# Kernel tuning notes

Measured on AMD Instinct MI355X. Metric: run time of the kernel, lower is better.

## Reference

```python
import jax, jax.numpy as jnp
import numpy as np

BN_EPS = 1e-5

def conv1d(x, w, b, pad):
    # x: (B, C_in, L), w: (C_out, C_in, K=4), stride 1
    y = jax.lax.conv_general_dilated(x, w, window_strides=(1,), padding=[(pad, pad)],
                                     dimension_numbers=('NCH', 'OIH', 'NCH'))
    return y + b[None, :, None]

def batchnorm_train(x, g, be):
    # training-mode BN over (N, L) per channel, biased variance (torch semantics)
    m = jnp.mean(x, axis=(0, 2), keepdims=True)
    v = jnp.mean((x - m) ** 2, axis=(0, 2), keepdims=True)
    return (x - m) * jax.lax.rsqrt(v + BN_EPS) * g[None, :, None] + be[None, :, None]

def setup_inputs() -> dict:
    key = jax.random.key(0)
    ks = jax.random.split(key, 12)
    B, T, C_in, E, K = 32, 4096, 12, 256, 1024
    d = {}
    d['x'] = jax.random.normal(ks[0], (B, T, C_in), jnp.float32)
    d['w1'] = jax.random.normal(ks[1], (E, C_in, 4), jnp.float32) * 0.1
    d['b1'] = jax.random.normal(ks[2], (E,), jnp.float32) * 0.1
    d['g1'] = jnp.ones((E,), jnp.float32); d['be1'] = jnp.zeros((E,), jnp.float32)
    d['w2'] = jax.random.normal(ks[3], (E, E, 4), jnp.float32) * 0.05
    d['b2'] = jax.random.normal(ks[4], (E,), jnp.float32) * 0.1
    d['g2'] = jnp.ones((E,), jnp.float32); d['be2'] = jnp.zeros((E,), jnp.float32)
    d['w3'] = jax.random.normal(ks[5], (E, E, 4), jnp.float32) * 0.05
    d['b3'] = jax.random.normal(ks[6], (E,), jnp.float32) * 0.1
    d['g3'] = jnp.ones((E,), jnp.float32); d['be3'] = jnp.zeros((E,), jnp.float32)
    d['w4'] = jax.random.normal(ks[7], (E, E, 4), jnp.float32) * 0.05
    d['b4'] = jax.random.normal(ks[8], (E,), jnp.float32) * 0.1
    d['codebook'] = jax.random.normal(ks[9], (K, E), jnp.float32)
    return d

def reference(x, w1, b1, g1, be1, w2, b2, g2, be2, w3, b3, g3, be3, w4, b4, codebook):
    h = jnp.transpose(x, (0, 2, 1))                 # (B, C, T)
    h = jax.nn.relu(batchnorm_train(conv1d(h, w1, b1, 2), g1, be1))  # (B,E,T+1)
    h = jax.nn.relu(batchnorm_train(conv1d(h, w2, b2, 1), g2, be2))  # (B,E,T)
    h = jax.nn.relu(batchnorm_train(conv1d(h, w3, b3, 2), g3, be3))  # (B,E,T+1)
    h = conv1d(h, w4, b4, 1)                                         # (B,E,T)
    z_e = jnp.transpose(h, (0, 2, 1))               # (B, T, E)
    # squared-L2 nearest codebook entry (argmin identical to cdist p=2)
    d2 = (jnp.sum(z_e ** 2, axis=-1, keepdims=True)
          - 2.0 * jnp.einsum('bte,ke->btk', z_e, codebook)
          + jnp.sum(codebook ** 2, axis=-1)[None, None, :])
    ids = jnp.argmin(d2, axis=-1)                   # (B, T) int
    z_q = codebook[ids]                             # gather (B, T, E)
    z_q = z_e + jax.lax.stop_gradient(z_q - z_e)    # straight-through
    return (z_e, z_q)
```

## Files before the change

### kernel.cpp

```cpp
#include <hip/hip_runtime.h>
#include <hip/hip_bf16.h>


#define B_   32
#define T_   4096
#define E_   256
#define CIN_ 12
#define LM_  4096

typedef __attribute__((ext_vector_type(4))) float f32x4;
typedef __attribute__((ext_vector_type(8))) short bf16x8;
typedef __attribute__((ext_vector_type(8))) unsigned short u16x8;

__device__ __forceinline__ unsigned int bf_rne(float v) {
  unsigned int u = __float_as_uint(v);
  return (u + 0x7fffu + ((u >> 16) & 1u)) >> 16;
}
__device__ __forceinline__ void split2(float v, unsigned short& h, unsigned short& l) {
  unsigned int hu = bf_rne(v);
  h = (unsigned short)hu;
  l = (unsigned short)bf_rne(v - __uint_as_float(hu << 16));
}
__device__ __forceinline__ void split3(float v, unsigned short& a,
                                       unsigned short& b, unsigned short& c) {
  unsigned int h = bf_rne(v);
  a = (unsigned short)h;
  float r1 = v - __uint_as_float(h << 16);
  unsigned int m = bf_rne(r1);
  b = (unsigned short)m;
  float r2 = r1 - __uint_as_float(m << 16);
  c = (unsigned short)bf_rne(r2);
}

__global__ __launch_bounds__(256) void prep_w_kernel(
    const float* __restrict__ w, unsigned short* __restrict__ wh,
    unsigned short* __restrict__ wm, unsigned short* __restrict__ wl) {
  const int g = blockIdx.x * 256 + threadIdx.x;
  const int coff  = g & 31;
  const int e     = (g >> 5) & 255;
  const int slice = g >> 13;
  const int cc = slice >> 2, kt = slice & 3;
  const int c = cc * 32 + coff;
  unsigned short h, m, l;
  split3(w[(size_t)e * 1024 + (size_t)c * 4 + kt], h, m, l);
  const size_t o = (size_t)slice * 8192 + (size_t)e * 32 + coff;
  wh[o] = h; wm[o] = m; wl[o] = l;
}

__global__ __launch_bounds__(256) void conv1_kernel(
    const float* __restrict__ x, const float* __restrict__ w1,
    const float* __restrict__ b1, float* __restrict__ out_main,
    float* __restrict__ out_tail) {
  __shared__ __align__(16) float xs[259][12];
  __shared__ __align__(16) float wsh[E_ * 48];
  __shared__ float bs[E_];
  const int tid = threadIdx.x;
  const int b = blockIdx.y;
  const int l0 = blockIdx.x * 256;
  for (int idx = tid; idx < 259 * 12; idx += 256) {
    int r = idx / 12, c = idx - r * 12;
    int t = l0 - 2 + r;
    xs[r][c] = (t >= 0 && t < T_) ? x[((size_t)b * T_ + t) * CIN_ + c] : 0.f;
  }
  for (int idx = tid; idx < E_ * 48; idx += 256) wsh[idx] = w1[idx];
  bs[tid] = b1[tid];
  __syncthreads();
  float xr[4][12];
  #pragma unroll
  for (int r = 0; r < 4; ++r)
    #pragma unroll
    for (int c = 0; c < 12; ++c) xr[r][c] = xs[tid + r][c];
  const int l = l0 + tid;
  for (int e = 0; e < E_; ++e) {
    float acc = bs[e];
    #pragma unroll
    for (int c = 0; c < 12; ++c) {
      const float4 wv = *(const float4*)&wsh[e * 48 + c * 4];
      acc += wv.x * xr[0][c] + wv.y * xr[1][c] + wv.z * xr[2][c] + wv.w * xr[3][c];
    }
    if (l < LM_)       out_main[((size_t)b * E_ + e) * LM_ + l] = acc;
    else if (l == LM_) out_tail[(size_t)b * E_ + e] = acc;
  }
}

__global__ __launch_bounds__(256) void bn_pass1(
    const float* __restrict__ hmain, const float* __restrict__ htail,
    float* __restrict__ psum, float* __restrict__ psq) {
  const int bx = blockIdx.x;
  const int c = bx >> 3, sl = bx & 7;
  const int tid = threadIdx.x;
  float s = 0.f, s2 = 0.f;
  for (int b = 0; b < B_; ++b) {
    const float* p = hmain + ((size_t)b * E_ + c) * LM_ + sl * 512;
    const float v0 = p[tid], v1 = p[tid + 256];
    s += v0 + v1;
    s2 += v0 * v0 + v1 * v1;
  }
  if (htail && sl == 7 && tid < B_) {
    const float v = htail[(size_t)tid * E_ + c];
    s += v; s2 += v * v;
  }
  __shared__ float sh[256], sh2[256];
  sh[tid] = s; sh2[tid] = s2; __syncthreads();
  for (int off = 128; off > 0; off >>= 1) {
    if (tid < off) { sh[tid] += sh[tid + off]; sh2[tid] += sh2[tid + off]; }
    __syncthreads();
  }
  if (tid == 0) { psum[bx] = sh[0]; psq[bx] = sh2[0]; }
}

__global__ __launch_bounds__(256) void bn_pass2(
    const float* __restrict__ psum, const float* __restrict__ psq,
    const float* __restrict__ g, const float* __restrict__ be,
    float* __restrict__ scale, float* __restrict__ shift, int hasTail) {
  const int c = threadIdx.x;
  double s = 0.0, s2 = 0.0;
  #pragma unroll
  for (int i = 0; i < 8; ++i) { s += psum[c * 8 + i]; s2 += psq[c * 8 + i]; }
  double N = (double)B_ * (double)(LM_ + hasTail);
  double m = s / N, var = s2 / N - m * m;
  double a = (double)g[c] / sqrt(var + 1e-5);
  scale[c] = (float)a;
  shift[c] = (float)((double)be[c] - m * a);
}

template <int MODE>
__global__ __launch_bounds__(256) void conv_mfma(
    const float* __restrict__ in_main, const float* __restrict__ in_tail,
    const unsigned short* __restrict__ wh, const unsigned short* __restrict__ wm,
    const unsigned short* __restrict__ wl, const float* __restrict__ bias,
    const float* __restrict__ scale, const float* __restrict__ shift,
    float* __restrict__ out, float* __restrict__ out_tail, int pad) {
  __shared__ __align__(16) char Xb[2][3][8448];
  __shared__ float sc_sh[E_], sf_sh[E_];
  const int tid = threadIdx.x, lane = tid & 63, wv = tid >> 6;
  const int q = lane >> 4, n16 = lane & 15;
  const int b = blockIdx.z, e0 = blockIdx.y * 128, l0 = blockIdx.x * 128;
  const int eB = e0 + (wv & 1) * 64;
  const int lB = (wv >> 1) * 64;
  sc_sh[tid] = scale[tid]; sf_sh[tid] = shift[tid];

  f32x4 acc[4][4];
  #pragma unroll
  for (int i = 0; i < 4; ++i)
    #pragma unroll
    for (int j = 0; j < 4; ++j) acc[i][j] = (f32x4){0.f, 0.f, 0.f, 0.f};

  const float* inb = in_main + (size_t)b * E_ * LM_;
  const float* intb = in_tail ? (in_tail + (size_t)b * E_) : nullptr;

  auto loadTask = [&](int idx, int cc, f32x4& va, f32x4& vb) {
    const int cp = idx & 15, uq = idx >> 4;
    const int c = cc * 32 + cp * 2;
    const int u0 = uq * 4;
    const int lb = l0 - pad + u0;
    const float* pa = inb + (size_t)c * LM_;
    const float* pb = pa + LM_;
    if (lb >= 0 && lb + 3 < LM_) {
      va = *(const f32x4*)(pa + lb);
      vb = *(const f32x4*)(pb + lb);
    } else {
      #pragma unroll
      for (int s = 0; s < 4; ++s) {
        const int l = lb + s;
        float oa = 0.f, ob = 0.f;
        if (l >= 0 && l < LM_)        { oa = pa[l]; ob = pb[l]; }
        else if (l == LM_ && intb)    { oa = intb[c]; ob = intb[c + 1]; }
        va[s] = oa; vb[s] = ob;
      }
    }
  };
  auto writeTask = [&](int idx, int cc, f32x4 va, f32x4 vb, int nb) {
    const int cp = idx & 15, uq = idx >> 4;
    const int c = cc * 32 + cp * 2;
    const int u0 = uq * 4;
    const int lb = l0 - pad + u0;
    const float sca = sc_sh[c], sfa = sf_sh[c];
    const float scb = sc_sh[c + 1], sfb = sf_sh[c + 1];
    const int cg = cp >> 2;
    const int cb4 = (cp & 3) * 4;
    #pragma unroll
    for (int s = 0; s < 4; ++s) {
      const int l = lb + s;
      const bool ok = (l >= 0) && (l < LM_ || (l == LM_ && intb));
      const float fa = ok ? fmaxf(fmaf(va[s], sca, sfa), 0.f) : 0.f;
      const float fb = ok ? fmaxf(fmaf(vb[s], scb, sfb), 0.f) : 0.f;
      unsigned short ha, ma, la, hb, mb, lb2;
      split3(fa, ha, ma, la);
      split3(fb, hb, mb, lb2);
      const int u = u0 + s;
      const int off = u * 64 + ((cg ^ ((u >> 1) & 3)) << 4) + cb4;
      *(unsigned int*)(Xb[nb][0] + off) = (unsigned int)ha | ((unsigned int)hb << 16);
      *(unsigned int*)(Xb[nb][1] + off) = (unsigned int)ma | ((unsigned int)mb << 16);
      *(unsigned int*)(Xb[nb][2] + off) = (unsigned int)la | ((unsigned int)lb2 << 16);
    }
  };

  __syncthreads();
  {
    f32x4 va, vb;
    #pragma unroll
    for (int s2 = 0; s2 < 3; ++s2) {
      const int idx = tid + s2 * 256;
      if (idx < 528) { loadTask(idx, 0, va, vb); writeTask(idx, 0, va, vb, 0); }
    }
  }
  __syncthreads();

  for (int cc = 0; cc < 8; ++cc) {
    const int cur = cc & 1;
    f32x4 pva[3], pvb[3];
    if (cc < 7) {
      #pragma unroll
      for (int s2 = 0; s2 < 3; ++s2) {
        const int idx = tid + s2 * 256;
        if (idx < 528) loadTask(idx, cc + 1, pva[s2], pvb[s2]);
      }
    }
    const char* XhB = Xb[cur][0];
    const char* XmB = Xb[cur][1];
    const char* XlB = Xb[cur][2];
    for (int kt = 0; kt < 4; ++kt) {
      bf16x8 Bh[4], Bm[4], Bl[4];
      #pragma unroll
      for (int ni = 0; ni < 4; ++ni) {
        const int u = lB + ni * 16 + n16 + kt;
        const int off = u * 64 + ((q ^ ((u >> 1) & 3)) << 4);
        Bh[ni] = *(const bf16x8*)(XhB + off);
        Bm[ni] = *(const bf16x8*)(XmB + off);
        Bl[ni] = *(const bf16x8*)(XlB + off);
      }
      const size_t so = (size_t)(cc * 4 + kt) * 8192 + (size_t)q * 8;
      #pragma unroll
      for (int mi = 0; mi < 4; ++mi) {
        const size_t o = so + (size_t)(eB + mi * 16 + n16) * 32;
        const bf16x8 Ah = *(const bf16x8*)(wh + o);
        const bf16x8 Am = *(const bf16x8*)(wm + o);
        const bf16x8 Al = *(const bf16x8*)(wl + o);
        #pragma unroll
        for (int ni = 0; ni < 4; ++ni) {
          acc[mi][ni] = __builtin_amdgcn_mfma_f32_16x16x32_bf16(Ah, Bh[ni], acc[mi][ni], 0, 0, 0);
          acc[mi][ni] = __builtin_amdgcn_mfma_f32_16x16x32_bf16(Ah, Bm[ni], acc[mi][ni], 0, 0, 0);
          acc[mi][ni] = __builtin_amdgcn_mfma_f32_16x16x32_bf16(Am, Bh[ni], acc[mi][ni], 0, 0, 0);
          acc[mi][ni] = __builtin_amdgcn_mfma_f32_16x16x32_bf16(Ah, Bl[ni], acc[mi][ni], 0, 0, 0);
          acc[mi][ni] = __builtin_amdgcn_mfma_f32_16x16x32_bf16(Al, Bh[ni], acc[mi][ni], 0, 0, 0);
          acc[mi][ni] = __builtin_amdgcn_mfma_f32_16x16x32_bf16(Am, Bm[ni], acc[mi][ni], 0, 0, 0);
        }
      }
    }
    if (cc < 7) {
      #pragma unroll
      for (int s2 = 0; s2 < 3; ++s2) {
        const int idx = tid + s2 * 256;
        if (idx < 528) writeTask(idx, cc + 1, pva[s2], pvb[s2], cur ^ 1);
      }
    }
    __syncthreads();
  }

  #pragma unroll
  for (int mi = 0; mi < 4; ++mi) {
    const int eb4 = eB + mi * 16 + q * 4;
    const f32x4 bv = *(const f32x4*)(bias + eb4);
    #pragma unroll
    for (int ni = 0; ni < 4; ++ni) {
      const int col = l0 + lB + ni * 16 + n16;
      const f32x4 r = acc[mi][ni] + bv;
      if constexpr (MODE == 0) {
        #pragma unroll
        for (int rr = 0; rr < 4; ++rr)
          out[((size_t)b * E_ + eb4 + rr) * LM_ + col] = r[rr];
      } else if constexpr (MODE == 1) {
        if (col < LM_) {
          #pragma unroll
          for (int rr = 0; rr < 4; ++rr)
            out[((size_t)b * E_ + eb4 + rr) * LM_ + col] = r[rr];
        } else if (col == LM_) {
          #pragma unroll
          for (int rr = 0; rr < 4; ++rr)
            out_tail[(size_t)b * E_ + eb4 + rr] = r[rr];
        }
      } else {
        #pragma unroll
        for (int rr = 0; rr < 4; ++rr)
          out[((size_t)b * T_ + col) * E_ + eb4 + rr] = r[rr];
      }
    }
  }
}

__global__ __launch_bounds__(256) void cbprep_kernel(
    const float* __restrict__ cb, unsigned short* __restrict__ cbh,
    unsigned short* __restrict__ cbl, float* __restrict__ cnh) {
  const int code = blockIdx.x * 4 + (threadIdx.x >> 6);
  const int lane = threadIdx.x & 63;
  const f32x4 v = *(const f32x4*)&cb[(size_t)code * E_ + lane * 4];
  ushort4 h, l;
  split2(v.x, h.x, l.x); split2(v.y, h.y, l.y);
  split2(v.z, h.z, l.z); split2(v.w, h.w, l.w);
  *(ushort4*)&cbh[(size_t)code * E_ + lane * 4] = h;
  *(ushort4*)&cbl[(size_t)code * E_ + lane * 4] = l;
  float s = v.x * v.x + v.y * v.y + v.z * v.z + v.w * v.w;
  for (int off = 32; off > 0; off >>= 1) s += __shfl_xor(s, off, 64);
  if (lane == 0) cnh[code] = 0.5f * s;
}

__global__ __launch_bounds__(256) void vq_mfma_kernel(
    const float* __restrict__ z, const unsigned short* __restrict__ cbh,
    const unsigned short* __restrict__ cbl, const float* __restrict__ cnh,
    int* __restrict__ ids) {
  __shared__ __align__(16) char cbLds[2][16384];
  __shared__ float cn_sh[1024];
  const int tid = threadIdx.x;
  const int lane = tid & 63;
  const int w = tid >> 6;
  const int q = lane >> 4;
  const int m15 = lane & 15;
  const int rbase = blockIdx.x * 128 + w * 32;
  for (int i = tid; i < 1024; i += 256) cn_sh[i] = cnh[i];

  const int sc0 = tid >> 5, sl0 = tid & 31;
  const int sc1 = (tid + 256) >> 5, sl1 = (tid + 256) & 31;
  const int d0 = sc0 * 512 + (((sl0 ^ (sc0 & 7))) << 4);
  const int d1 = sc1 * 512 + (((sl1 ^ (sc1 & 7))) << 4);
  const u16x8* srcH = (const u16x8*)cbh;
  const u16x8* srcL = (const u16x8*)cbl;

  {
    u16x8 h0 = srcH[tid], h1 = srcH[tid + 256];
    u16x8 l0 = srcL[tid], l1 = srcL[tid + 256];
    *(u16x8*)(cbLds[0] + d0) = h0;
    *(u16x8*)(cbLds[0] + d1) = h1;
    *(u16x8*)(cbLds[0] + 8192 + d0) = l0;
    *(u16x8*)(cbLds[0] + 8192 + d1) = l1;
  }

  bf16x8 zh[2][8], zl[2][8];
  #pragma unroll
  for (int g = 0; g < 2; ++g) {
    const int row = rbase + g * 16 + m15;
    const float* zr = z + (size_t)row * 256 + q * 8;
    #pragma unroll
    for (int ec = 0; ec < 8; ++ec) {
      const f32x4 v0 = *(const f32x4*)(zr + ec * 32);
      const f32x4 v1 = *(const f32x4*)(zr + ec * 32 + 4);
      u16x8 h, l;
      #pragma unroll
      for (int j = 0; j < 4; ++j) {
        unsigned short a, b;
        split2(v0[j], a, b); h[j] = a; l[j] = b;
        split2(v1[j], a, b); h[4 + j] = a; l[4 + j] = b;
      }
      zh[g][ec] = (bf16x8)h;
      zl[g][ec] = (bf16x8)l;
    }
  }
  __syncthreads();

  float best[2] = {-3.4e38f, -3.4e38f};
  int bidx[2] = {0, 0};
  const int swz = (m15 & 7) << 4;
  const int rowOff = m15 * 512;

  for (int cg = 0; cg < 64; ++cg) {
    const int cur = cg & 1;
    u16x8 ph0, ph1, pl0, pl1;
    if (cg < 63) {
      const int sb = (cg + 1) * 512;
      ph0 = srcH[sb + tid]; ph1 = srcH[sb + tid + 256];
      pl0 = srcL[sb + tid]; pl1 = srcL[sb + tid + 256];
    }
    const char* baseH = cbLds[cur];
    const char* baseL = cbLds[cur] + 8192;
    f32x4 ahh[2], ahl[2], alh[2];
    #pragma unroll
    for (int g = 0; g < 2; ++g) {
      ahh[g] = (f32x4){0.f, 0.f, 0.f, 0.f};
      ahl[g] = (f32x4){0.f, 0.f, 0.f, 0.f};
      alh[g] = (f32x4){0.f, 0.f, 0.f, 0.f};
    }
    #pragma unroll
    for (int ec = 0; ec < 8; ++ec) {
      const int co = rowOff + ((q * 16 + ec * 64) ^ swz);
      const bf16x8 Ah = *(const bf16x8*)(baseH + co);
      const bf16x8 Al = *(const bf16x8*)(baseL + co);
      #pragma unroll
      for (int g = 0; g < 2; ++g) {
        ahh[g] = __builtin_amdgcn_mfma_f32_16x16x32_bf16(Ah, zh[g][ec], ahh[g], 0, 0, 0);
        ahl[g] = __builtin_amdgcn_mfma_f32_16x16x32_bf16(Ah, zl[g][ec], ahl[g], 0, 0, 0);
        alh[g] = __builtin_amdgcn_mfma_f32_16x16x32_bf16(Al, zh[g][ec], alh[g], 0, 0, 0);
      }
    }
    const f32x4 cn = *(const f32x4*)&cn_sh[cg * 16 + q * 4];
    #pragma unroll
    for (int g = 0; g < 2; ++g) {
      #pragma unroll
      for (int r = 0; r < 4; ++r) {
        const float s = (ahh[g][r] + ahl[g][r]) + alh[g][r] - cn[r];
        const int code = cg * 16 + q * 4 + r;
        if (s > best[g]) { best[g] = s; bidx[g] = code; }
      }
    }
    if (cg < 63) {
      char* nb = cbLds[cur ^ 1];
      *(u16x8*)(nb + d0) = ph0;
      *(u16x8*)(nb + d1) = ph1;
      *(u16x8*)(nb + 8192 + d0) = pl0;
      *(u16x8*)(nb + 8192 + d1) = pl1;
    }
    __syncthreads();
  }

  #pragma unroll
  for (int g = 0; g < 2; ++g) {
    #pragma unroll
    for (int off = 16; off <= 32; off <<= 1) {
      const float ov = __shfl_xor(best[g], off, 64);
      const int oi = __shfl_xor(bidx[g], off, 64);
      if (ov > best[g] || (ov == best[g] && oi < bidx[g])) { best[g] = ov; bidx[g] = oi; }
    }
  }
  if (q == 0) {
    #pragma unroll
    for (int g = 0; g < 2; ++g) ids[rbase + g * 16 + lane] = bidx[g];
  }
}

__global__ __launch_bounds__(256) void gather_kernel(
    const int* __restrict__ ids, const float* __restrict__ cb,
    float* __restrict__ zq) {
  const int row = blockIdx.x * 4 + (threadIdx.x >> 6);
  const int lane = threadIdx.x & 63;
  const int id = ids[row];
  const float4 v = *(const float4*)&cb[(size_t)id * E_ + lane * 4];
  *(float4*)&zq[(size_t)row * E_ + lane * 4] = v;
}

extern "C" void kernel_launch(void* const* d_in, const int* in_sizes, int n_in,
                              void* d_out, int out_size, void* d_ws, size_t ws_size,
                              hipStream_t stream) {
  const float* x   = (const float*)d_in[0];
  const float* w1  = (const float*)d_in[1];
  const float* b1  = (const float*)d_in[2];
  const float* g1  = (const float*)d_in[3];
  const float* be1 = (const float*)d_in[4];
  const float* w2  = (const float*)d_in[5];
  const float* b2  = (const float*)d_in[6];
  const float* g2  = (const float*)d_in[7];
  const float* be2 = (const float*)d_in[8];
  const float* w3  = (const float*)d_in[9];
  const float* b3  = (const float*)d_in[10];
  const float* g3  = (const float*)d_in[11];
  const float* be3 = (const float*)d_in[12];
  const float* w4  = (const float*)d_in[13];
  const float* b4  = (const float*)d_in[14];
  const float* cb  = (const float*)d_in[15];

  char* ws = (char*)d_ws;
  float* tailA  = (float*)(ws);
  float* scale1 = (float*)(ws + 40960);  float* shift1 = (float*)(ws + 45056);
  float* scale2 = (float*)(ws + 49152);  float* shift2 = (float*)(ws + 53248);
  float* scale3 = (float*)(ws + 57344);  float* shift3 = (float*)(ws + 61440);
  float* cnh    = (float*)(ws + 65536);
  float* psum   = (float*)(ws + 73728);
  float* psq    = (float*)(ws + 81920);
  int*   ids    = (int*)(ws + 131072);
  const size_t MB = 1u << 20;
  unsigned short* wh2 = (unsigned short*)(ws + MB);
  unsigned short* wm2 = (unsigned short*)(ws + MB + 524288u);
  unsigned short* wl2 = (unsigned short*)(ws + MB + 1048576u);
  unsigned short* wh3 = (unsigned short*)(ws + MB + 1572864u);
  unsigned short* wm3 = (unsigned short*)(ws + MB + 2097152u);
  unsigned short* wl3 = (unsigned short*)(ws + MB + 2621440u);
  unsigned short* wh4 = (unsigned short*)(ws + MB + 3145728u);
  unsigned short* wm4 = (unsigned short*)(ws + MB + 3670016u);
  unsigned short* wl4 = (unsigned short*)(ws + MB + 4194304u);

  float* half1 = (float*)d_out;
  float* half2 = half1 + (size_t)33554432;
  unsigned short* cbh = (unsigned short*)half2;
  unsigned short* cbl = (unsigned short*)half2 + 262144;

  prep_w_kernel<<<1024, 256, 0, stream>>>(w2, wh2, wm2, wl2);
  prep_w_kernel<<<1024, 256, 0, stream>>>(w3, wh3, wm3, wl3);
  prep_w_kernel<<<1024, 256, 0, stream>>>(w4, wh4, wm4, wl4);

  conv1_kernel<<<dim3(17, 32), 256, 0, stream>>>(x, w1, b1, half2, tailA);
  bn_pass1<<<2048, 256, 0, stream>>>(half2, tailA, psum, psq);
  bn_pass2<<<1, 256, 0, stream>>>(psum, psq, g1, be1, scale1, shift1, 1);
  conv_mfma<0><<<dim3(32, 2, 32), 256, 0, stream>>>(half2, tailA, wh2, wm2, wl2, b2,
                                                    scale1, shift1, half1, nullptr, 1);
  bn_pass1<<<2048, 256, 0, stream>>>(half1, nullptr, psum, psq);
  bn_pass2<<<1, 256, 0, stream>>>(psum, psq, g2, be2, scale2, shift2, 0);
  conv_mfma<1><<<dim3(33, 2, 32), 256, 0, stream>>>(half1, nullptr, wh3, wm3, wl3, b3,
                                                    scale2, shift2, half2, tailA, 2);
  bn_pass1<<<2048, 256, 0, stream>>>(half2, tailA, psum, psq);
  bn_pass2<<<1, 256, 0, stream>>>(psum, psq, g3, be3, scale3, shift3, 1);
  conv_mfma<2><<<dim3(32, 2, 32), 256, 0, stream>>>(half2, tailA, wh4, wm4, wl4, b4,
                                                    scale3, shift3, half1, nullptr, 1);
  cbprep_kernel<<<256, 256, 0, stream>>>(cb, cbh, cbl, cnh);
  vq_mfma_kernel<<<1024, 256, 0, stream>>>(half1, cbh, cbl, cnh, ids);
  gather_kernel<<<32768, 256, 0, stream>>>(ids, cb, half2);
}
```

Baseline: 1.649 ms.

## Retile conv MFMA blocks to cover all 256 channels over 64 positions

Each conv block now computes all 256 output channels for a 64-wide time tile, with each of the four waves owning 64 channels, instead of 128 channels by 128 positions. This removes the duplicated input staging and BN/split3 conversion across the two channel blocks, since the 3-way bf16 split of activations is done once per time tile. It also halves the LDS footprint for the input buffers. In exchange, the weight fetches are no longer shared across a 128-wide time tile, so weight traffic per output column roughly doubles.

```diff
diff --git a/kernel.cpp b/kernel.cpp
--- a/kernel.cpp
+++ b/kernel.cpp
@@ -131,13 +131,12 @@
     const unsigned short* __restrict__ wl, const float* __restrict__ bias,
     const float* __restrict__ scale, const float* __restrict__ shift,
     float* __restrict__ out, float* __restrict__ out_tail, int pad) {
-  __shared__ __align__(16) char Xb[2][3][8448];
+  __shared__ __align__(16) char Xbuf[2][3][4352];
   __shared__ float sc_sh[E_], sf_sh[E_];
   const int tid = threadIdx.x, lane = tid & 63, wv = tid >> 6;
   const int q = lane >> 4, n16 = lane & 15;
-  const int b = blockIdx.z, e0 = blockIdx.y * 128, l0 = blockIdx.x * 128;
-  const int eB = e0 + (wv & 1) * 64;
-  const int lB = (wv >> 1) * 64;
+  const int b = blockIdx.z, l0 = blockIdx.x * 64;
+  const int eB = wv * 64;
   sc_sh[tid] = scale[tid]; sf_sh[tid] = shift[tid];
 
   f32x4 acc[4][4];
@@ -190,41 +189,40 @@
       split3(fb, hb, mb, lb2);
       const int u = u0 + s;
       const int off = u * 64 + ((cg ^ ((u >> 1) & 3)) << 4) + cb4;
-      *(unsigned int*)(Xb[nb][0] + off) = (unsigned int)ha | ((unsigned int)hb << 16);
-      *(unsigned int*)(Xb[nb][1] + off) = (unsigned int)ma | ((unsigned int)mb << 16);
-      *(unsigned int*)(Xb[nb][2] + off) = (unsigned int)la | ((unsigned int)lb2 << 16);
+      *(unsigned int*)(Xbuf[nb][0] + off) = (unsigned int)ha | ((unsigned int)hb << 16);
+      *(unsigned int*)(Xbuf[nb][1] + off) = (unsigned int)ma | ((unsigned int)mb << 16);
+      *(unsigned int*)(Xbuf[nb][2] + off) = (unsigned int)la | ((unsigned int)lb2 << 16);
     }
   };
 
   __syncthreads();
   {
     f32x4 va, vb;
-    #pragma unroll
-    for (int s2 = 0; s2 < 3; ++s2) {
-      const int idx = tid + s2 * 256;
-      if (idx < 528) { loadTask(idx, 0, va, vb); writeTask(idx, 0, va, vb, 0); }
+    loadTask(tid, 0, va, vb);
+    writeTask(tid, 0, va, vb, 0);
+    if (tid < 16) {
+      f32x4 vc, vd;
+      loadTask(256 + tid, 0, vc, vd);
+      writeTask(256 + tid, 0, vc, vd, 0);
     }
   }
   __syncthreads();
 
   for (int cc = 0; cc < 8; ++cc) {
     const int cur = cc & 1;
-    f32x4 pva[3], pvb[3];
+    f32x4 va0, vb0, va1, vb1;
     if (cc < 7) {
-      #pragma unroll
-      for (int s2 = 0; s2 < 3; ++s2) {
-        const int idx = tid + s2 * 256;
-        if (idx < 528) loadTask(idx, cc + 1, pva[s2], pvb[s2]);
-      }
-    }
-    const char* XhB = Xb[cur][0];
-    const char* XmB = Xb[cur][1];
-    const char* XlB = Xb[cur][2];
+      loadTask(tid, cc + 1, va0, vb0);
+      if (tid < 16) loadTask(256 + tid, cc + 1, va1, vb1);
+    }
+    const char* XhB = Xbuf[cur][0];
+    const char* XmB = Xbuf[cur][1];
+    const char* XlB = Xbuf[cur][2];
     for (int kt = 0; kt < 4; ++kt) {
       bf16x8 Bh[4], Bm[4], Bl[4];
       #pragma unroll
       for (int ni = 0; ni < 4; ++ni) {
-        const int u = lB + ni * 16 + n16 + kt;
+        const int u = ni * 16 + n16 + kt;
         const int off = u * 64 + ((q ^ ((u >> 1) & 3)) << 4);
         Bh[ni] = *(const bf16x8*)(XhB + off);
         Bm[ni] = *(const bf16x8*)(XmB + off);
@@ -249,11 +247,8 @@
       }
     }
     if (cc < 7) {
-      #pragma unroll
-      for (int s2 = 0; s2 < 3; ++s2) {
-        const int idx = tid + s2 * 256;
-        if (idx < 528) writeTask(idx, cc + 1, pva[s2], pvb[s2], cur ^ 1);
-      }
+      writeTask(tid, cc + 1, va0, vb0, cur ^ 1);
+      if (tid < 16) writeTask(256 + tid, cc + 1, va1, vb1, cur ^ 1);
     }
     __syncthreads();
   }
@@ -264,7 +259,7 @@
     const f32x4 bv = *(const f32x4*)(bias + eb4);
     #pragma unroll
     for (int ni = 0; ni < 4; ++ni) {
-      const int col = l0 + lB + ni * 16 + n16;
+      const int col = l0 + ni * 16 + n16;
       const f32x4 r = acc[mi][ni] + bv;
       if constexpr (MODE == 0) {
         #pragma unroll
@@ -488,15 +483,15 @@
   conv1_kernel<<<dim3(17, 32), 256, 0, stream>>>(x, w1, b1, half2, tailA);
   bn_pass1<<<2048, 256, 0, stream>>>(half2, tailA, psum, psq);
   bn_pass2<<<1, 256, 0, stream>>>(psum, psq, g1, be1, scale1, shift1, 1);
-  conv_mfma<0><<<dim3(32, 2, 32), 256, 0, stream>>>(half2, tailA, wh2, wm2, wl2, b2,
+  conv_mfma<0><<<dim3(64, 1, 32), 256, 0, stream>>>(half2, tailA, wh2, wm2, wl2, b2,
                                                     scale1, shift1, half1, nullptr, 1);
   bn_pass1<<<2048, 256, 0, stream>>>(half1, nullptr, psum, psq);
   bn_pass2<<<1, 256, 0, stream>>>(psum, psq, g2, be2, scale2, shift2, 0);
-  conv_mfma<1><<<dim3(33, 2, 32), 256, 0, stream>>>(half1, nullptr, wh3, wm3, wl3, b3,
+  conv_mfma<1><<<dim3(65, 1, 32), 256, 0, stream>>>(half1, nullptr, wh3, wm3, wl3, b3,
                                                     scale2, shift2, half2, tailA, 2);
   bn_pass1<<<2048, 256, 0, stream>>>(half2, tailA, psum, psq);
   bn_pass2<<<1, 256, 0, stream>>>(psum, psq, g3, be3, scale3, shift3, 1);
-  conv_mfma<2><<<dim3(32, 2, 32), 256, 0, stream>>>(half2, tailA, wh4, wm4, wl4, b4,
+  conv_mfma<2><<<dim3(64, 1, 32), 256, 0, stream>>>(half2, tailA, wh4, wm4, wl4, b4,
                                                     scale3, shift3, half1, nullptr, 1);
   cbprep_kernel<<<256, 256, 0, stream>>>(cb, cbh, cbl, cnh);
   vq_mfma_kernel<<<1024, 256, 0, stream>>>(half1, cbh, cbl, cnh, ids);
```

After: 2.468 ms. 1.5x slower.
